# Kernel optimization log

Hardware: AMD Instinct MI355X
Metric: run time of the kernel (lower is better)

The kernel has to match this reference:

```python
import jax, jax.numpy as jnp
import numpy as np

RANGES = (1, 2, 4, 10, 25)
B, L, D, V = 64, 1000, 300, 50000  # L divisible by every r in RANGES -> no remainder group


def setup_inputs() -> dict:
    key = jax.random.key(0)
    ks = jax.random.split(key, 12)
    u = lambda k, s: jax.random.uniform(k, s, dtype=jnp.float32) / 6  # matches torch.rand(...)/6
    return {
        "article_in": jax.random.randint(ks[0], (B, L), 0, V),
        "emb": jax.random.normal(ks[1], (V, D), dtype=jnp.float32) * 0.02,
        "w_ce": u(ks[2], (len(RANGES), D, D)),   # per-range W in contract-expand
        "b_ce": u(ks[3], (len(RANGES), 1, D)),   # per-range b (shape (1,D) in source)
        "w1": u(ks[4], (3, len(RANGES))),
        "b1": u(ks[5], (3, D)),
        "w2": u(ks[6], (1, 3)),
        "b2": u(ks[7], (1, D)),
        "wz": u(ks[8], (D, D)),
        "bz": u(ks[9], (1, D)),
        "wo": u(ks[10], (D, D)),
        "bo": u(ks[11], (1, D)),
    }


def _mru(x, w_ce, b_ce, w1, b1, w2, b2, wz, bz, wo, bo):
    b, l, d = x.shape
    # --- contract-expand: segment-sum windows of size r, tiny matmul, broadcast back /r ---
    ce = []
    for i, r in enumerate(RANGES):
        seg = x.reshape(b, l // r, r, d).sum(axis=2)                 # [B, L/r, D] segment sums
        t = jax.nn.relu(seg @ w_ce[i]) + b_ce[i]                     # relu(sum @ W) + b
        ce.append(jnp.repeat(t, r, axis=1) / r)                      # expand each group back, divided by r
    pre = jnp.stack(ce, axis=2)                                      # [B, L, 5, D]
    # --- multi-ranged reasoning MLP across the 5 ranges ---
    h1 = jax.nn.relu(jnp.einsum('ts,blsd->bltd', w1, pre) + b1)      # [B, L, 3, D]
    gate = jax.nn.relu(jnp.einsum('ot,bltd->blod', w2, h1) + b2)[:, :, 0, :]  # [B, L, D]
    # --- gated recurrent encoding (note: bias added OUTSIDE tanh, per source) ---
    z = jnp.tanh(x @ wz) + bz                                        # [B, L, D]
    o = jnp.tanh(x @ wo) + bo                                        # [B, L, D]

    def step(c, inp):
        g, zt, ot = inp
        c = g * c + (1.0 - g) * zt
        return c, ot * c

    seq = (gate.transpose(1, 0, 2), z.transpose(1, 0, 2), o.transpose(1, 0, 2))  # [L, B, D]
    _, h = jax.lax.scan(step, jnp.zeros((b, d), x.dtype), seq)
    return h.transpose(1, 0, 2)                                      # [B, L, D]


def reference(article_in, emb, w_ce, b_ce, w1, b1, w2, b2, wz, bz, wo, bo):
    x = emb[article_in]                                              # embedding lookup [B, L, D]
    return _mru(x, w_ce, b_ce, w1, b1, w2, b2, wz, bz, wo, bo)
```

## Files before the change

### kernel.cpp

```cpp
#include <hip/hip_runtime.h>
#include <hip/hip_bf16.h>

typedef unsigned short u16;
typedef unsigned int   u32;
typedef __attribute__((ext_vector_type(8))) short short8;
typedef __attribute__((ext_vector_type(4))) float floatx4;
typedef __attribute__((ext_vector_type(4))) unsigned short u16x4;

__device__ __forceinline__ u16 f2bf(float f){
  u32 x = __float_as_uint(f);
  u32 r = (x + 0x7fffu + ((x >> 16) & 1u)) >> 16;
  return (u16)r;
}
__device__ __forceinline__ float bf2f(u16 u){
  return __uint_as_float(((u32)u) << 16);
}
__device__ __forceinline__ float tanh_fast(float x){
  float xs = fminf(fmaxf(x, -16.f), 16.f);
  float e  = __builtin_amdgcn_exp2f(xs * 2.8853900817779268f);
  return (e - 1.f) * __builtin_amdgcn_rcpf(e + 1.f);
}
__device__ __forceinline__ void gload16(const void* g, void* l){
  __builtin_amdgcn_global_load_lds(
      (const __attribute__((address_space(1))) unsigned int*)g,
      (__attribute__((address_space(3))) unsigned int*)l, 16, 0, 0);
}

__global__ void k_gather4(const int* __restrict__ idx, const float* __restrict__ emb,
                          u16* __restrict__ x, int total){
  int i = blockIdx.x * blockDim.x + threadIdx.x;
  if (i >= total) return;
  int row = i / 80; int j = i - row * 80;
  u16x4 o;
  if (j < 75){
    const float4 v = *(const float4*)(emb + (size_t)idx[row] * 300 + j * 4);
    o[0] = f2bf(v.x); o[1] = f2bf(v.y); o[2] = f2bf(v.z); o[3] = f2bf(v.w);
  } else {
    o[0] = 0; o[1] = 0; o[2] = 0; o[3] = 0;
  }
  *(u16x4*)(x + (size_t)row * 320 + j * 4) = o;
}

__global__ void k_segsum_all(const u16* __restrict__ x,
                             u16* __restrict__ s2, u16* __restrict__ s4,
                             u16* __restrict__ s10, u16* __restrict__ s25, int total){
  int i = blockIdx.x * blockDim.x + threadIdx.x;
  if (i >= total) return;
  int d4 = i % 80; int rest = i / 80; int w = rest % 10; int b = rest / 10;
  const int dcol = d4 * 4;
  const u16* src = x + ((size_t)(b * 1000 + w * 100) * 320 + dcol);
  float a2[4] = {0,0,0,0}, a4[4] = {0,0,0,0}, a10[4] = {0,0,0,0}, a25[4] = {0,0,0,0};
  #pragma unroll
  for (int l = 0; l < 100; l++){
    u16x4 v = *(const u16x4*)(src + (size_t)l * 320);
    #pragma unroll
    for (int q = 0; q < 4; q++){
      float f = bf2f(v[q]);
      a2[q] += f; a4[q] += f; a10[q] += f; a25[q] += f;
    }
    if ((l & 1) == 1){
      u16x4 o;
      #pragma unroll
      for (int q = 0; q < 4; q++){ o[q] = f2bf(a2[q]); a2[q] = 0.f; }
      *(u16x4*)(s2 + ((size_t)(b * 500 + w * 50 + (l >> 1)) * 320 + dcol)) = o;
    }
    if ((l & 3) == 3){
      u16x4 o;
      #pragma unroll
      for (int q = 0; q < 4; q++){ o[q] = f2bf(a4[q]); a4[q] = 0.f; }
      *(u16x4*)(s4 + ((size_t)(b * 250 + w * 25 + (l >> 2)) * 320 + dcol)) = o;
    }
    if (l % 10 == 9){
      u16x4 o;
      #pragma unroll
      for (int q = 0; q < 4; q++){ o[q] = f2bf(a10[q]); a10[q] = 0.f; }
      *(u16x4*)(s10 + ((size_t)(b * 100 + w * 10 + l / 10) * 320 + dcol)) = o;
    }
    if (l % 25 == 24){
      u16x4 o;
      #pragma unroll
      for (int q = 0; q < 4; q++){ o[q] = f2bf(a25[q]); a25[q] = 0.f; }
      *(u16x4*)(s25 + ((size_t)(b * 40 + w * 4 + l / 25) * 320 + dcol)) = o;
    }
  }
}

__global__ void k_wprep(const float* __restrict__ wce, const float* __restrict__ wz,
                        const float* __restrict__ wo, u16* __restrict__ wT, int total){
  int i = blockIdx.x * blockDim.x + threadIdx.x;
  if (i >= total) return;
  int mat = i / 102400; int rem = i - mat * 102400;
  int n = rem / 320;    int k = rem - n * 320;
  float v = 0.f;
  if (n < 300 && k < 300){
    const float* src = (mat < 5) ? (wce + mat * 90000) : (mat == 5 ? wz : wo);
    v = src[k * 300 + n];
  }
  wT[i] = f2bf(v);
}

__global__ __launch_bounds__(512, 2) void k_gemm_all(
    const u16* __restrict__ x,  const u16* __restrict__ s2,
    const u16* __restrict__ s4, const u16* __restrict__ s10,
    const u16* __restrict__ s25,const u16* __restrict__ wT,
    u16* __restrict__ t0, u16* __restrict__ t1, u16* __restrict__ t2,
    u16* __restrict__ t3, u16* __restrict__ t4,
    u16* __restrict__ zb, u16* __restrict__ ob,
    const float* __restrict__ b_ce, const float* __restrict__ bz,
    const float* __restrict__ bo)
{
  __shared__ __align__(16) char lds[114688];

  const int bid = blockIdx.x;
  const u16 *A, *BT; u16* C; const float* bias;
  int mode; float scale; long tileRow;
  if (bid < 1512){
    const int xcd = bid & 7, j = bid >> 3;
    const int T = (j / 3) * 8 + xcd, m = j % 3;
    if (T >= 500) return;
    tileRow = (long)T * 128; A = x;
    if (m == 0)      { BT = wT;              C = t0; bias = b_ce; mode = 0; scale = 1.f; }
    else if (m == 1) { BT = wT + 5 * 102400; C = zb; bias = bz;   mode = 1; scale = 1.f; }
    else             { BT = wT + 6 * 102400; C = ob; bias = bo;   mode = 1; scale = 1.f; }
  } else {
    const int g = bid - 1512;
    if (g < 250)      { A=s2;  BT=wT+1*102400; C=t1; bias=b_ce+300;  mode=0; scale=0.5f;  tileRow=(long)g*128; }
    else if (g < 375) { A=s4;  BT=wT+2*102400; C=t2; bias=b_ce+600;  mode=0; scale=0.25f; tileRow=(long)(g-250)*128; }
    else if (g < 425) { A=s10; BT=wT+3*102400; C=t3; bias=b_ce+900;  mode=0; scale=0.1f;  tileRow=(long)(g-375)*128; }
    else              { A=s25; BT=wT+4*102400; C=t4; bias=b_ce+1200; mode=0; scale=0.04f; tileRow=(long)(g-425)*128; }
  }

  const int tid  = threadIdx.x;
  const int lane = tid & 63;
  const int wid  = tid >> 6;
  const int wr   = wid >> 2;
  const int wc   = wid & 3;

  const u16* aSrc[2]; int aDst[2];
  #pragma unroll
  for (int l = 0; l < 2; l++){
    const int idx = l * 512 + tid, row = idx >> 3, c = idx & 7;
    aSrc[l] = A + (tileRow + row) * 320 + ((c ^ (row & 7)) << 3);
    aDst[l] = (l * 512 + wid * 64) * 16;
  }
  const u16* bSrc[5]; int bDst[5];
  #pragma unroll
  for (int l = 0; l < 5; l++){
    const int idx = l * 512 + tid, col = idx >> 3, c = idx & 7;
    bSrc[l] = BT + col * 320 + ((c ^ (col & 7)) << 3);
    bDst[l] = (l * 512 + wid * 64) * 16;
  }

  const int rA  = wr * 64 + (lane & 15);
  const int cBt = wc * 80 + (lane & 15);
  int ksw[2];
  #pragma unroll
  for (int s = 0; s < 2; s++)
    ksw[s] = ((s * 4 + (lane >> 4)) ^ (lane & 7)) << 4;

  floatx4 acc[4][5];
  #pragma unroll
  for (int m = 0; m < 4; m++)
    #pragma unroll
    for (int n = 0; n < 5; n++)
      #pragma unroll
      for (int q = 0; q < 4; q++) acc[m][n][q] = 0.f;

  #pragma unroll
  for (int l = 0; l < 2; l++) gload16(aSrc[l], lds + aDst[l]);
  #pragma unroll
  for (int l = 0; l < 5; l++) gload16(bSrc[l], lds + 32768 + bDst[l]);
  __syncthreads();

  #pragma unroll
  for (int t = 0; t < 5; t++){
    const int cur = t & 1;
    if (t < 4){
      const int nb = cur ^ 1;
      #pragma unroll
      for (int l = 0; l < 2; l++) gload16(aSrc[l] + (t + 1) * 64, lds + nb * 16384 + aDst[l]);
      #pragma unroll
      for (int l = 0; l < 5; l++) gload16(bSrc[l] + (t + 1) * 64, lds + 32768 + nb * 40960 + bDst[l]);
    }
    const char* bA = lds + cur * 16384;
    const char* bB = lds + 32768 + cur * 40960;
    #pragma unroll
    for (int s = 0; s < 2; s++){
      short8 af[4], bf[5];
      #pragma unroll
      for (int m = 0; m < 4; m++)
        af[m] = *(const short8*)(bA + (rA + m * 16) * 128 + ksw[s]);
      #pragma unroll
      for (int n = 0; n < 5; n++)
        bf[n] = *(const short8*)(bB + (cBt + n * 16) * 128 + ksw[s]);
      #pragma unroll
      for (int m = 0; m < 4; m++)
        #pragma unroll
        for (int n = 0; n < 5; n++)
          acc[m][n] = __builtin_amdgcn_mfma_f32_16x16x32_bf16(af[m], bf[n], acc[m][n], 0, 0, 0);
    }
    __syncthreads();
  }

  const int colbase = wc * 80 + (lane & 15);
  const long rowb   = tileRow + wr * 64 + ((lane >> 4) << 2);
  #pragma unroll
  for (int m = 0; m < 4; m++){
    #pragma unroll
    for (int n = 0; n < 5; n++){
      const int gcol = colbase + n * 16;
      if (gcol < 300){
        const float bv = bias[gcol];
        #pragma unroll
        for (int r = 0; r < 4; r++){
          const long grow = rowb + m * 16 + r;
          float v = acc[m][n][r];
          v = (mode == 0) ? (fmaxf(v, 0.f) + bv) * scale : tanh_fast(v) + bv;
          C[grow * 300 + gcol] = f2bf(v);
        }
      }
    }
  }
}

__device__ __forceinline__ float gate_eval(
    float p0, float p1, float p2, float p3, float p4,
    const float W1[3][5], const float W2[3], const float B1[3], float B2)
{
  float acc2 = B2;
  #pragma unroll
  for (int t = 0; t < 3; t++){
    float u = W1[t][0]*p0 + W1[t][1]*p1 + W1[t][2]*p2 + W1[t][3]*p3 + W1[t][4]*p4 + B1[t];
    acc2 += W2[t] * fmaxf(u, 0.f);
  }
  return fmaxf(acc2, 0.f);
}

__global__ void k_scan1(const u16* __restrict__ t0, const u16* __restrict__ t1,
    const u16* __restrict__ t2, const u16* __restrict__ t3, const u16* __restrict__ t4,
    const u16* __restrict__ z,
    const float* __restrict__ w1, const float* __restrict__ b1,
    const float* __restrict__ w2, const float* __restrict__ b2,
    float* __restrict__ cA, float* __restrict__ cB, int total)
{
  int i = blockIdx.x * blockDim.x + threadIdx.x;
  if (i >= total) return;
  int d4 = i % 75; int rest = i / 75; int ch = rest % 20; int b = rest / 20;
  const int d = d4 * 4;
  float W1[3][5], W2[3], B1[3][4], B2[4];
  #pragma unroll
  for (int t = 0; t < 3; t++){
    #pragma unroll
    for (int s = 0; s < 5; s++) W1[t][s] = w1[t * 5 + s];
    W2[t] = w2[t];
    #pragma unroll
    for (int q = 0; q < 4; q++) B1[t][q] = b1[t * 300 + d + q];
  }
  #pragma unroll
  for (int q = 0; q < 4; q++) B2[q] = b2[d + q];
  float Ac[4] = {1.f,1.f,1.f,1.f}, Bc[4] = {0.f,0.f,0.f,0.f};
  const int l0 = ch * 50;
  for (int l = l0; l < l0 + 50; l++){
    u16x4 v0 = *(const u16x4*)(t0 + (size_t)(b * 1000 + l)        * 300 + d);
    u16x4 v1 = *(const u16x4*)(t1 + (size_t)(b * 500  + (l >> 1)) * 300 + d);
    u16x4 v2 = *(const u16x4*)(t2 + (size_t)(b * 250  + (l >> 2)) * 300 + d);
    u16x4 v3 = *(const u16x4*)(t3 + (size_t)(b * 100  + l / 10)   * 300 + d);
    u16x4 v4 = *(const u16x4*)(t4 + (size_t)(b * 40   + l / 25)   * 300 + d);
    u16x4 vz = *(const u16x4*)(z  + (size_t)(b * 1000 + l)        * 300 + d);
    #pragma unroll
    for (int q = 0; q < 4; q++){
      float B1q[3] = {B1[0][q], B1[1][q], B1[2][q]};
      float g  = gate_eval(bf2f(v0[q]), bf2f(v1[q]), bf2f(v2[q]), bf2f(v3[q]), bf2f(v4[q]),
                           W1, W2, B1q, B2[q]);
      Ac[q] = g * Ac[q];
      Bc[q] = g * Bc[q] + (1.f - g) * bf2f(vz[q]);
    }
  }
  *(float4*)(cA + (size_t)ch * 19200 + b * 300 + d) = make_float4(Ac[0], Ac[1], Ac[2], Ac[3]);
  *(float4*)(cB + (size_t)ch * 19200 + b * 300 + d) = make_float4(Bc[0], Bc[1], Bc[2], Bc[3]);
}

__global__ void k_scan2(const float* __restrict__ cA, const float* __restrict__ cB,
                        float* __restrict__ cinit, int total){
  int i = blockIdx.x * blockDim.x + threadIdx.x;
  if (i >= total) return;
  float c = 0.f;
  for (int ch = 0; ch < 20; ch++){
    cinit[ch * 19200 + i] = c;
    c = cA[ch * 19200 + i] * c + cB[ch * 19200 + i];
  }
}

__global__ void k_scan3(const u16* __restrict__ t0, const u16* __restrict__ t1,
    const u16* __restrict__ t2, const u16* __restrict__ t3, const u16* __restrict__ t4,
    const u16* __restrict__ z, const u16* __restrict__ o,
    const float* __restrict__ cinit,
    const float* __restrict__ w1, const float* __restrict__ b1,
    const float* __restrict__ w2, const float* __restrict__ b2,
    float* __restrict__ out, int total)
{
  int i = blockIdx.x * blockDim.x + threadIdx.x;
  if (i >= total) return;
  int d4 = i % 75; int rest = i / 75; int ch = rest % 20; int b = rest / 20;
  const int d = d4 * 4;
  float W1[3][5], W2[3], B1[3][4], B2[4];
  #pragma unroll
  for (int t = 0; t < 3; t++){
    #pragma unroll
    for (int s = 0; s < 5; s++) W1[t][s] = w1[t * 5 + s];
    W2[t] = w2[t];
    #pragma unroll
    for (int q = 0; q < 4; q++) B1[t][q] = b1[t * 300 + d + q];
  }
  #pragma unroll
  for (int q = 0; q < 4; q++) B2[q] = b2[d + q];
  float c[4];
  {
    float4 ci = *(const float4*)(cinit + (size_t)ch * 19200 + b * 300 + d);
    c[0] = ci.x; c[1] = ci.y; c[2] = ci.z; c[3] = ci.w;
  }
  const int l0 = ch * 50;
  for (int l = l0; l < l0 + 50; l++){
    u16x4 v0 = *(const u16x4*)(t0 + (size_t)(b * 1000 + l)        * 300 + d);
    u16x4 v1 = *(const u16x4*)(t1 + (size_t)(b * 500  + (l >> 1)) * 300 + d);
    u16x4 v2 = *(const u16x4*)(t2 + (size_t)(b * 250  + (l >> 2)) * 300 + d);
    u16x4 v3 = *(const u16x4*)(t3 + (size_t)(b * 100  + l / 10)   * 300 + d);
    u16x4 v4 = *(const u16x4*)(t4 + (size_t)(b * 40   + l / 25)   * 300 + d);
    u16x4 vz = *(const u16x4*)(z  + (size_t)(b * 1000 + l)        * 300 + d);
    u16x4 vo = *(const u16x4*)(o  + (size_t)(b * 1000 + l)        * 300 + d);
    float4 res;
    #pragma unroll
    for (int q = 0; q < 4; q++){
      float B1q[3] = {B1[0][q], B1[1][q], B1[2][q]};
      float g  = gate_eval(bf2f(v0[q]), bf2f(v1[q]), bf2f(v2[q]), bf2f(v3[q]), bf2f(v4[q]),
                           W1, W2, B1q, B2[q]);
      c[q] = g * c[q] + (1.f - g) * bf2f(vz[q]);
      ((float*)&res)[q] = bf2f(vo[q]) * c[q];
    }
    *(float4*)(out + (size_t)(b * 1000 + l) * 300 + d) = res;
  }
}

extern "C" void kernel_launch(void* const* d_in, const int* in_sizes, int n_in,
                              void* d_out, int out_size, void* d_ws, size_t ws_size,
                              hipStream_t stream){
  const int*   article = (const int*)  d_in[0];
  const float* emb     = (const float*)d_in[1];
  const float* w_ce    = (const float*)d_in[2];
  const float* b_ce    = (const float*)d_in[3];
  const float* w1      = (const float*)d_in[4];
  const float* b1      = (const float*)d_in[5];
  const float* w2      = (const float*)d_in[6];
  const float* b2      = (const float*)d_in[7];
  const float* wz      = (const float*)d_in[8];
  const float* bz      = (const float*)d_in[9];
  const float* wo      = (const float*)d_in[10];
  const float* bo      = (const float*)d_in[11];
  float* out = (float*)d_out;
  char*  ws  = (char*)d_ws;

  u16* x    = (u16*)(ws + 0UL);
  u16* s2   = (u16*)(ws + 40960000UL);
  u16* s4   = (u16*)(ws + 61440000UL);
  u16* s10  = (u16*)(ws + 71680000UL);
  u16* s25  = (u16*)(ws + 75776000UL);
  u16* wT   = (u16*)(ws + 77414400UL);
  u16* t0   = (u16*)(ws + 78848000UL);
  u16* t1   = (u16*)(ws + 117248000UL);
  u16* t2   = (u16*)(ws + 136448000UL);
  u16* t3   = (u16*)(ws + 146048000UL);
  u16* t4   = (u16*)(ws + 149888000UL);
  u16* zb   = (u16*)(ws + 151424000UL);
  u16* ob   = (u16*)(ws + 189824000UL);
  float* cA = (float*)(ws + 228224000UL);
  float* cB = (float*)(ws + 229760000UL);
  float* ci = (float*)(ws + 231296000UL);
  (void)ws_size; (void)in_sizes; (void)n_in; (void)out_size;

  k_wprep  <<< 2800, 256, 0, stream>>>(w_ce, wz, wo, wT, 716800);
  k_gather4<<<20000, 256, 0, stream>>>(article, emb, x, 64000 * 80);
  k_segsum_all<<<200, 256, 0, stream>>>(x, s2, s4, s10, s25, 51200);

  k_gemm_all<<<1957, 512, 0, stream>>>(x, s2, s4, s10, s25, wT,
                                       t0, t1, t2, t3, t4, zb, ob,
                                       b_ce, bz, bo);

  k_scan1<<<375, 256, 0, stream>>>(t0, t1, t2, t3, t4, zb, w1, b1, w2, b2, cA, cB, 96000);
  k_scan2<<< 75, 256, 0, stream>>>(cA, cB, ci, 19200);
  k_scan3<<<375, 256, 0, stream>>>(t0, t1, t2, t3, t4, zb, ob, ci, w1, b1, w2, b2, out, 96000);
}
```

Baseline: 254.3 us.

## Fuse segment sums into gather, shrink GEMM tiles, double scan chunk count

The embedding gather now also produces the range-2, 4 and 10 segment sums from the fp32 values, and a separate small kernel computes the range-25 sums. The GEMM moves from 128-row tiles with 512 threads and a 64-wide K step to 64-row tiles with 256 threads and a 32-wide K step, using less LDS so more blocks and waves can fit. The chunked scan goes from 20 to 40 chunks per sequence with the range-25 term hoisted out of the loop, and its scratch buffers are moved into the now-unused segsum region. These changes target low occupancy and the extra pass over x, at the cost of more K iterations and barriers in the GEMM, more scan blocks, and workspace aliasing that must stay valid.

```diff
diff --git a/kernel.cpp b/kernel.cpp
--- a/kernel.cpp
+++ b/kernel.cpp
@@ -26,63 +26,65 @@
       (__attribute__((address_space(3))) unsigned int*)l, 16, 0, 0);
 }
 
-__global__ void k_gather4(const int* __restrict__ idx, const float* __restrict__ emb,
-                          u16* __restrict__ x, int total){
-  int i = blockIdx.x * blockDim.x + threadIdx.x;
-  if (i >= total) return;
-  int row = i / 80; int j = i - row * 80;
+__global__ void k_gather_seg(const int* __restrict__ idx, const float* __restrict__ emb,
+                             u16* __restrict__ x, u16* __restrict__ s2,
+                             u16* __restrict__ s4, u16* __restrict__ s10, int total){
+  int i = blockIdx.x * blockDim.x + threadIdx.x;
+  if (i >= total) return;
+  int d4 = i % 80; int rest = i / 80; int w = rest % 50; int b = rest / 50;
+  const int dcol = d4 * 4;
+  const int r0 = b * 1000 + w * 20;
+  float a2[4] = {0,0,0,0}, a4[4] = {0,0,0,0}, a10[4] = {0,0,0,0};
+  #pragma unroll
+  for (int j = 0; j < 20; j++){
+    const int r = r0 + j;
+    u16x4 o; o[0] = 0; o[1] = 0; o[2] = 0; o[3] = 0;
+    if (d4 < 75){
+      const float4 v = *(const float4*)(emb + (size_t)idx[r] * 300 + dcol);
+      o[0] = f2bf(v.x); o[1] = f2bf(v.y); o[2] = f2bf(v.z); o[3] = f2bf(v.w);
+      a2[0] += v.x; a2[1] += v.y; a2[2] += v.z; a2[3] += v.w;
+      a4[0] += v.x; a4[1] += v.y; a4[2] += v.z; a4[3] += v.w;
+      a10[0] += v.x; a10[1] += v.y; a10[2] += v.z; a10[3] += v.w;
+    }
+    *(u16x4*)(x + (size_t)r * 320 + dcol) = o;
+    if (j & 1){
+      u16x4 s; 
+      #pragma unroll
+      for (int q = 0; q < 4; q++){ s[q] = f2bf(a2[q]); a2[q] = 0.f; }
+      *(u16x4*)(s2 + ((size_t)(b * 500 + w * 10 + (j >> 1)) * 320 + dcol)) = s;
+    }
+    if ((j & 3) == 3){
+      u16x4 s;
+      #pragma unroll
+      for (int q = 0; q < 4; q++){ s[q] = f2bf(a4[q]); a4[q] = 0.f; }
+      *(u16x4*)(s4 + ((size_t)(b * 250 + w * 5 + (j >> 2)) * 320 + dcol)) = s;
+    }
+    if (j == 9 || j == 19){
+      u16x4 s;
+      #pragma unroll
+      for (int q = 0; q < 4; q++){ s[q] = f2bf(a10[q]); a10[q] = 0.f; }
+      *(u16x4*)(s10 + ((size_t)(b * 100 + w * 2 + j / 10) * 320 + dcol)) = s;
+    }
+  }
+}
+
+__global__ void k_s25(const u16* __restrict__ x, u16* __restrict__ s25, int total){
+  int i = blockIdx.x * blockDim.x + threadIdx.x;
+  if (i >= total) return;
+  int d4 = i % 80; int rest = i / 80; int g = rest % 40; int b = rest / 40;
+  const int dcol = d4 * 4;
+  const u16* src = x + ((size_t)(b * 1000 + g * 25) * 320 + dcol);
+  float a[4] = {0,0,0,0};
+  #pragma unroll
+  for (int j = 0; j < 25; j++){
+    u16x4 v = *(const u16x4*)(src + (size_t)j * 320);
+    #pragma unroll
+    for (int q = 0; q < 4; q++) a[q] += bf2f(v[q]);
+  }
   u16x4 o;
-  if (j < 75){
-    const float4 v = *(const float4*)(emb + (size_t)idx[row] * 300 + j * 4);
-    o[0] = f2bf(v.x); o[1] = f2bf(v.y); o[2] = f2bf(v.z); o[3] = f2bf(v.w);
-  } else {
-    o[0] = 0; o[1] = 0; o[2] = 0; o[3] = 0;
-  }
-  *(u16x4*)(x + (size_t)row * 320 + j * 4) = o;
-}
-
-__global__ void k_segsum_all(const u16* __restrict__ x,
-                             u16* __restrict__ s2, u16* __restrict__ s4,
-                             u16* __restrict__ s10, u16* __restrict__ s25, int total){
-  int i = blockIdx.x * blockDim.x + threadIdx.x;
-  if (i >= total) return;
-  int d4 = i % 80; int rest = i / 80; int w = rest % 10; int b = rest / 10;
-  const int dcol = d4 * 4;
-  const u16* src = x + ((size_t)(b * 1000 + w * 100) * 320 + dcol);
-  float a2[4] = {0,0,0,0}, a4[4] = {0,0,0,0}, a10[4] = {0,0,0,0}, a25[4] = {0,0,0,0};
-  #pragma unroll
-  for (int l = 0; l < 100; l++){
-    u16x4 v = *(const u16x4*)(src + (size_t)l * 320);
-    #pragma unroll
-    for (int q = 0; q < 4; q++){
-      float f = bf2f(v[q]);
-      a2[q] += f; a4[q] += f; a10[q] += f; a25[q] += f;
-    }
-    if ((l & 1) == 1){
-      u16x4 o;
-      #pragma unroll
-      for (int q = 0; q < 4; q++){ o[q] = f2bf(a2[q]); a2[q] = 0.f; }
-      *(u16x4*)(s2 + ((size_t)(b * 500 + w * 50 + (l >> 1)) * 320 + dcol)) = o;
-    }
-    if ((l & 3) == 3){
-      u16x4 o;
-      #pragma unroll
-      for (int q = 0; q < 4; q++){ o[q] = f2bf(a4[q]); a4[q] = 0.f; }
-      *(u16x4*)(s4 + ((size_t)(b * 250 + w * 25 + (l >> 2)) * 320 + dcol)) = o;
-    }
-    if (l % 10 == 9){
-      u16x4 o;
-      #pragma unroll
-      for (int q = 0; q < 4; q++){ o[q] = f2bf(a10[q]); a10[q] = 0.f; }
-      *(u16x4*)(s10 + ((size_t)(b * 100 + w * 10 + l / 10) * 320 + dcol)) = o;
-    }
-    if (l % 25 == 24){
-      u16x4 o;
-      #pragma unroll
-      for (int q = 0; q < 4; q++){ o[q] = f2bf(a25[q]); a25[q] = 0.f; }
-      *(u16x4*)(s25 + ((size_t)(b * 40 + w * 4 + l / 25) * 320 + dcol)) = o;
-    }
-  }
+  #pragma unroll
+  for (int q = 0; q < 4; q++) o[q] = f2bf(a[q]);
+  *(u16x4*)(s25 + ((size_t)(b * 40 + g) * 320 + dcol)) = o;
 }
 
 __global__ void k_wprep(const float* __restrict__ wce, const float* __restrict__ wz,
@@ -99,7 +101,7 @@
   wT[i] = f2bf(v);
 }
 
-__global__ __launch_bounds__(512, 2) void k_gemm_all(
+__global__ __launch_bounds__(256, 3) void k_gemm_all(
     const u16* __restrict__ x,  const u16* __restrict__ s2,
     const u16* __restrict__ s4, const u16* __restrict__ s10,
     const u16* __restrict__ s25,const u16* __restrict__ wT,
@@ -109,54 +111,43 @@
     const float* __restrict__ b_ce, const float* __restrict__ bz,
     const float* __restrict__ bo)
 {
-  __shared__ __align__(16) char lds[114688];
+  __shared__ __align__(16) char lds[49152];
 
   const int bid = blockIdx.x;
   const u16 *A, *BT; u16* C; const float* bias;
   int mode; float scale; long tileRow;
-  if (bid < 1512){
+  if (bid < 3000){
     const int xcd = bid & 7, j = bid >> 3;
     const int T = (j / 3) * 8 + xcd, m = j % 3;
-    if (T >= 500) return;
-    tileRow = (long)T * 128; A = x;
+    tileRow = (long)T * 64; A = x;
     if (m == 0)      { BT = wT;              C = t0; bias = b_ce; mode = 0; scale = 1.f; }
     else if (m == 1) { BT = wT + 5 * 102400; C = zb; bias = bz;   mode = 1; scale = 1.f; }
     else             { BT = wT + 6 * 102400; C = ob; bias = bo;   mode = 1; scale = 1.f; }
   } else {
-    const int g = bid - 1512;
-    if (g < 250)      { A=s2;  BT=wT+1*102400; C=t1; bias=b_ce+300;  mode=0; scale=0.5f;  tileRow=(long)g*128; }
-    else if (g < 375) { A=s4;  BT=wT+2*102400; C=t2; bias=b_ce+600;  mode=0; scale=0.25f; tileRow=(long)(g-250)*128; }
-    else if (g < 425) { A=s10; BT=wT+3*102400; C=t3; bias=b_ce+900;  mode=0; scale=0.1f;  tileRow=(long)(g-375)*128; }
-    else              { A=s25; BT=wT+4*102400; C=t4; bias=b_ce+1200; mode=0; scale=0.04f; tileRow=(long)(g-425)*128; }
+    const int g = bid - 3000;
+    if (g < 500)      { A=s2;  BT=wT+1*102400; C=t1; bias=b_ce+300;  mode=0; scale=0.5f;  tileRow=(long)g*64; }
+    else if (g < 750) { A=s4;  BT=wT+2*102400; C=t2; bias=b_ce+600;  mode=0; scale=0.25f; tileRow=(long)(g-500)*64; }
+    else if (g < 850) { A=s10; BT=wT+3*102400; C=t3; bias=b_ce+900;  mode=0; scale=0.1f;  tileRow=(long)(g-750)*64; }
+    else              { A=s25; BT=wT+4*102400; C=t4; bias=b_ce+1200; mode=0; scale=0.04f; tileRow=(long)(g-850)*64; }
   }
 
   const int tid  = threadIdx.x;
   const int lane = tid & 63;
   const int wid  = tid >> 6;
-  const int wr   = wid >> 2;
-  const int wc   = wid & 3;
-
-  const u16* aSrc[2]; int aDst[2];
-  #pragma unroll
-  for (int l = 0; l < 2; l++){
-    const int idx = l * 512 + tid, row = idx >> 3, c = idx & 7;
-    aSrc[l] = A + (tileRow + row) * 320 + ((c ^ (row & 7)) << 3);
-    aDst[l] = (l * 512 + wid * 64) * 16;
-  }
-  const u16* bSrc[5]; int bDst[5];
+
+  const int arow = tid >> 2, ac = tid & 3;
+  const u16* aSrc = A + (tileRow + arow) * 320 + ((ac ^ ((arow >> 1) & 3)) << 3);
+  const u16* bSrc[5];
   #pragma unroll
   for (int l = 0; l < 5; l++){
-    const int idx = l * 512 + tid, col = idx >> 3, c = idx & 7;
-    bSrc[l] = BT + col * 320 + ((c ^ (col & 7)) << 3);
-    bDst[l] = (l * 512 + wid * 64) * 16;
-  }
-
-  const int rA  = wr * 64 + (lane & 15);
-  const int cBt = wc * 80 + (lane & 15);
-  int ksw[2];
-  #pragma unroll
-  for (int s = 0; s < 2; s++)
-    ksw[s] = ((s * 4 + (lane >> 4)) ^ (lane & 7)) << 4;
+    const int idx2 = l * 256 + tid, col = idx2 >> 2, cc = idx2 & 3;
+    bSrc[l] = BT + col * 320 + ((cc ^ ((col >> 1) & 3)) << 3);
+  }
+  const int wbase = wid * 1024;
+
+  const int rA  = lane & 15;
+  const int cBt = wid * 80 + (lane & 15);
+  const int kchunk = ((lane >> 4) ^ ((lane >> 1) & 3)) << 4;
 
   floatx4 acc[4][5];
   #pragma unroll
@@ -166,44 +157,40 @@
       #pragma unroll
       for (int q = 0; q < 4; q++) acc[m][n][q] = 0.f;
 
-  #pragma unroll
-  for (int l = 0; l < 2; l++) gload16(aSrc[l], lds + aDst[l]);
-  #pragma unroll
-  for (int l = 0; l < 5; l++) gload16(bSrc[l], lds + 32768 + bDst[l]);
+  gload16(aSrc, lds + wbase);
+  #pragma unroll
+  for (int l = 0; l < 5; l++) gload16(bSrc[l], lds + 8192 + l * 4096 + wbase);
   __syncthreads();
 
   #pragma unroll
-  for (int t = 0; t < 5; t++){
+  for (int t = 0; t < 10; t++){
     const int cur = t & 1;
-    if (t < 4){
+    if (t < 9){
       const int nb = cur ^ 1;
-      #pragma unroll
-      for (int l = 0; l < 2; l++) gload16(aSrc[l] + (t + 1) * 64, lds + nb * 16384 + aDst[l]);
-      #pragma unroll
-      for (int l = 0; l < 5; l++) gload16(bSrc[l] + (t + 1) * 64, lds + 32768 + nb * 40960 + bDst[l]);
-    }
-    const char* bA = lds + cur * 16384;
-    const char* bB = lds + 32768 + cur * 40960;
-    #pragma unroll
-    for (int s = 0; s < 2; s++){
-      short8 af[4], bf[5];
-      #pragma unroll
-      for (int m = 0; m < 4; m++)
-        af[m] = *(const short8*)(bA + (rA + m * 16) * 128 + ksw[s]);
+      gload16(aSrc + (t + 1) * 32, lds + nb * 4096 + wbase);
+      #pragma unroll
+      for (int l = 0; l < 5; l++)
+        gload16(bSrc[l] + (t + 1) * 32, lds + 8192 + nb * 20480 + l * 4096 + wbase);
+    }
+    const char* bA = lds + cur * 4096;
+    const char* bB = lds + 8192 + cur * 20480;
+    short8 af[4], bf[5];
+    #pragma unroll
+    for (int m = 0; m < 4; m++)
+      af[m] = *(const short8*)(bA + (rA + m * 16) * 64 + kchunk);
+    #pragma unroll
+    for (int n = 0; n < 5; n++)
+      bf[n] = *(const short8*)(bB + (cBt + n * 16) * 64 + kchunk);
+    #pragma unroll
+    for (int m = 0; m < 4; m++)
       #pragma unroll
       for (int n = 0; n < 5; n++)
-        bf[n] = *(const short8*)(bB + (cBt + n * 16) * 128 + ksw[s]);
-      #pragma unroll
-      for (int m = 0; m < 4; m++)
-        #pragma unroll
-        for (int n = 0; n < 5; n++)
-          acc[m][n] = __builtin_amdgcn_mfma_f32_16x16x32_bf16(af[m], bf[n], acc[m][n], 0, 0, 0);
-    }
+        acc[m][n] = __builtin_amdgcn_mfma_f32_16x16x32_bf16(af[m], bf[n], acc[m][n], 0, 0, 0);
     __syncthreads();
   }
 
-  const int colbase = wc * 80 + (lane & 15);
-  const long rowb   = tileRow + wr * 64 + ((lane >> 4) << 2);
+  const int colbase = wid * 80 + (lane & 15);
+  const long rowb   = tileRow + ((lane >> 4) << 2);
   #pragma unroll
   for (int m = 0; m < 4; m++){
     #pragma unroll
@@ -245,7 +232,7 @@
 {
   int i = blockIdx.x * blockDim.x + threadIdx.x;
   if (i >= total) return;
-  int d4 = i % 75; int rest = i / 75; int ch = rest % 20; int b = rest / 20;
+  int d4 = i % 75; int rest = i / 75; int ch = rest % 40; int b = rest / 40;
   const int d = d4 * 4;
   float W1[3][5], W2[3], B1[3][4], B2[4];
   #pragma unroll
@@ -259,13 +246,13 @@
   #pragma unroll
   for (int q = 0; q < 4; q++) B2[q] = b2[d + q];
   float Ac[4] = {1.f,1.f,1.f,1.f}, Bc[4] = {0.f,0.f,0.f,0.f};
-  const int l0 = ch * 50;
-  for (int l = l0; l < l0 + 50; l++){
+  const int l0 = ch * 25;
+  const u16x4 v4 = *(const u16x4*)(t4 + (size_t)(b * 40 + ch) * 300 + d);
+  for (int l = l0; l < l0 + 25; l++){
     u16x4 v0 = *(const u16x4*)(t0 + (size_t)(b * 1000 + l)        * 300 + d);
     u16x4 v1 = *(const u16x4*)(t1 + (size_t)(b * 500  + (l >> 1)) * 300 + d);
     u16x4 v2 = *(const u16x4*)(t2 + (size_t)(b * 250  + (l >> 2)) * 300 + d);
     u16x4 v3 = *(const u16x4*)(t3 + (size_t)(b * 100  + l / 10)   * 300 + d);
-    u16x4 v4 = *(const u16x4*)(t4 + (size_t)(b * 40   + l / 25)   * 300 + d);
     u16x4 vz = *(const u16x4*)(z  + (size_t)(b * 1000 + l)        * 300 + d);
     #pragma unroll
     for (int q = 0; q < 4; q++){
@@ -285,7 +272,7 @@
   int i = blockIdx.x * blockDim.x + threadIdx.x;
   if (i >= total) return;
   float c = 0.f;
-  for (int ch = 0; ch < 20; ch++){
+  for (int ch = 0; ch < 40; ch++){
     cinit[ch * 19200 + i] = c;
     c = cA[ch * 19200 + i] * c + cB[ch * 19200 + i];
   }
@@ -301,7 +288,7 @@
 {
   int i = blockIdx.x * blockDim.x + threadIdx.x;
   if (i >= total) return;
-  int d4 = i % 75; int rest = i / 75; int ch = rest % 20; int b = rest / 20;
+  int d4 = i % 75; int rest = i / 75; int ch = rest % 40; int b = rest / 40;
   const int d = d4 * 4;
   float W1[3][5], W2[3], B1[3][4], B2[4];
   #pragma unroll
@@ -319,13 +306,13 @@
     float4 ci = *(const float4*)(cinit + (size_t)ch * 19200 + b * 300 + d);
     c[0] = ci.x; c[1] = ci.y; c[2] = ci.z; c[3] = ci.w;
   }
-  const int l0 = ch * 50;
-  for (int l = l0; l < l0 + 50; l++){
+  const int l0 = ch * 25;
+  const u16x4 v4 = *(const u16x4*)(t4 + (size_t)(b * 40 + ch) * 300 + d);
+  for (int l = l0; l < l0 + 25; l++){
     u16x4 v0 = *(const u16x4*)(t0 + (size_t)(b * 1000 + l)        * 300 + d);
     u16x4 v1 = *(const u16x4*)(t1 + (size_t)(b * 500  + (l >> 1)) * 300 + d);
     u16x4 v2 = *(const u16x4*)(t2 + (size_t)(b * 250  + (l >> 2)) * 300 + d);
     u16x4 v3 = *(const u16x4*)(t3 + (size_t)(b * 100  + l / 10)   * 300 + d);
-    u16x4 v4 = *(const u16x4*)(t4 + (size_t)(b * 40   + l / 25)   * 300 + d);
     u16x4 vz = *(const u16x4*)(z  + (size_t)(b * 1000 + l)        * 300 + d);
     u16x4 vo = *(const u16x4*)(o  + (size_t)(b * 1000 + l)        * 300 + d);
     float4 res;
@@ -372,20 +359,20 @@
   u16* t4   = (u16*)(ws + 149888000UL);
   u16* zb   = (u16*)(ws + 151424000UL);
   u16* ob   = (u16*)(ws + 189824000UL);
-  float* cA = (float*)(ws + 228224000UL);
-  float* cB = (float*)(ws + 229760000UL);
-  float* ci = (float*)(ws + 231296000UL);
+  float* cA = (float*)(ws + 40960000UL);
+  float* cB = (float*)(ws + 44032000UL);
+  float* ci = (float*)(ws + 47104000UL);
   (void)ws_size; (void)in_sizes; (void)n_in; (void)out_size;
 
-  k_wprep  <<< 2800, 256, 0, stream>>>(w_ce, wz, wo, wT, 716800);
-  k_gather4<<<20000, 256, 0, stream>>>(article, emb, x, 64000 * 80);
-  k_segsum_all<<<200, 256, 0, stream>>>(x, s2, s4, s10, s25, 51200);
-
-  k_gemm_all<<<1957, 512, 0, stream>>>(x, s2, s4, s10, s25, wT,
+  k_wprep     <<<2800, 256, 0, stream>>>(w_ce, wz, wo, wT, 716800);
+  k_gather_seg<<<1000, 256, 0, stream>>>(article, emb, x, s2, s4, s10, 256000);
+  k_s25       <<< 800, 256, 0, stream>>>(x, s25, 204800);
+
+  k_gemm_all<<<3890, 256, 0, stream>>>(x, s2, s4, s10, s25, wT,
                                        t0, t1, t2, t3, t4, zb, ob,
                                        b_ce, bz, bo);
 
-  k_scan1<<<375, 256, 0, stream>>>(t0, t1, t2, t3, t4, zb, w1, b1, w2, b2, cA, cB, 96000);
+  k_scan1<<<750, 256, 0, stream>>>(t0, t1, t2, t3, t4, zb, w1, b1, w2, b2, cA, cB, 192000);
   k_scan2<<< 75, 256, 0, stream>>>(cA, cB, ci, 19200);
-  k_scan3<<<375, 256, 0, stream>>>(t0, t1, t2, t3, t4, zb, ob, ci, w1, b1, w2, b2, out, 96000);
-}
+  k_scan3<<<750, 256, 0, stream>>>(t0, t1, t2, t3, t4, zb, ob, ci, w1, b1, w2, b2, out, 192000);
+}
```

Result: faster. 240.8 us (-5.3%).
